# Performance work log

Hardware: AMD Instinct MI355X
Metric: run time of the kernel (lower is better)

The kernel has to match this reference:

```python
import jax, jax.numpy as jnp
import numpy as np

LEVELS = 16
BASE_RES = 16.0
MAX_RES = 2048.0
MAX_PARAMS = 2 ** 19
FEAT = 2
LOG_B = np.log(MAX_RES / BASE_RES) / (LEVELS - 1)
PRIMES = np.array([1, 2654435761, 805459861], dtype=np.uint32)


def level_meta():
    # Replays HashEncoder.__init__ offset/size bookkeeping.
    offsets, sizes, ress = [], [], []
    offset = 0
    begin_fast = LEVELS
    for i in range(LEVELS):
        res = int(np.ceil(BASE_RES * np.exp(i * LOG_B) - 1.0) + 1)  # grid_resolution
        full = float(res) ** 3
        aligned = int((full + 7) / 8) * 8  # align_to(full, 8)
        size = int(min(MAX_PARAMS, aligned))
        if full > size and begin_fast == LEVELS:
            begin_fast = i
        offsets.append(offset)
        sizes.append(size)
        ress.append(res)
        offset += size
    return offsets, sizes, ress, begin_fast, offset


OFFSETS, SIZES, RESS, BEGIN_FAST, TOTAL = level_meta()


def setup_inputs():
    key = jax.random.key(0)
    k1, k2 = jax.random.split(key)
    B = 2_000_000
    positions = jax.random.uniform(k1, (B, 3), dtype=jnp.float32)  # xyz in [0,1)
    table = jax.random.uniform(k2, (TOTAL, FEAT), dtype=jnp.float32,
                               minval=-1e-4, maxval=1e-4)
    return {"positions": positions, "table": table}


def _encode(positions, table):
    outs = []
    for level in range(LEVELS):  # fixed small structural loop (16 levels)
        scale = np.float32(BASE_RES * np.exp(level * LOG_B) - 1.0)  # grid_scale
        res = RESS[level]
        pos = positions * scale + 0.5          # [B,3]
        grid_f = jnp.floor(pos)
        frac = pos - grid_f                    # [B,3] trilinear fractions
        grid = grid_f.astype(jnp.uint32)
        acc = jnp.zeros((positions.shape[0], FEAT), dtype=jnp.float32)
        for corner in range(8):                # 8 cube corners (static unroll)
            sel = np.array([(corner >> d) & 1 for d in range(3)], dtype=np.uint32)
            pg = grid + sel                    # [B,3] uint32 corner coords
            w = jnp.prod(jnp.where(sel.astype(bool), frac, 1.0 - frac), axis=-1)  # [B]
            if level < BEGIN_FAST:
                # dense 'under_hash': x + y*res + z*res^2 (uint32 wraparound ok)
                strides = np.array([1, res, res * res], dtype=np.uint32)
                h = jnp.sum(pg * strides, axis=-1, dtype=jnp.uint32)
            else:
                # spatial 'fast_hash': xor of coord*prime with uint32 wraparound
                h = (pg[:, 0] * PRIMES[0]) ^ (pg[:, 1] * PRIMES[1]) ^ (pg[:, 2] * PRIMES[2])
            idx = (h % np.uint32(SIZES[level])).astype(jnp.int32) + OFFSETS[level]
            acc = acc + w[:, None] * table[idx]  # irregular gather [B,FEAT]
        outs.append(acc)
    # matches output_embedding[i, level].view(-1, levels*feat): level-major, feat inner
    return jnp.concatenate(outs, axis=-1)  # [B, LEVELS*FEAT]


def reference(positions, table):
    return _encode(positions, table)
```

## Files before the change

kernel.cpp:

```cpp
#include <hip/hip_runtime.h>
#include <math.h>

#define NLEVELS 16
#define BEGIN_FAST 5
#define P2 2654435761u
#define P3 805459861u
#define FAST_MASK 524287u
#define DENSE_TOTAL 330952u

constexpr unsigned kRes[NLEVELS] = {16u, 23u, 31u, 43u, 59u, 81u, 112u, 154u, 213u, 295u, 407u, 562u, 777u, 1073u, 1483u, 2048u};
constexpr unsigned kSize[NLEVELS] = {
    4096u, 12168u, 29792u, 79512u, 205384u,
    524288u, 524288u, 524288u, 524288u, 524288u, 524288u,
    524288u, 524288u, 524288u, 524288u, 524288u};
constexpr unsigned kOffset[NLEVELS] = {
    0u,       4096u,    16264u,   46056u,   125568u,  330952u,
    855240u,  1379528u, 1903816u, 2428104u, 2952392u, 3476680u,
    4000968u, 4525256u, 5049544u, 5573832u};

struct Scales {
    float s[NLEVELS];
};

typedef float fvec2 __attribute__((ext_vector_type(2)));
typedef float fvec4 __attribute__((ext_vector_type(4)));
typedef unsigned uvec4 __attribute__((ext_vector_type(4)));

__device__ __forceinline__ unsigned bfpack(float a, float b) {
    unsigned ua = __float_as_uint(a);
    unsigned ub = __float_as_uint(b);
    ua = (ua + 0x7FFFu + ((ua >> 16) & 1u)) >> 16;
    ub = (ub + 0x7FFFu + ((ub >> 16) & 1u)) & 0xFFFF0000u;
    return ua | ub;
}
__device__ __forceinline__ float bf_lo(unsigned e) { return __uint_as_float(e << 16); }
__device__ __forceinline__ float bf_hi(unsigned e) { return __uint_as_float(e & 0xFFFF0000u); }

__global__ __launch_bounds__(256) void convert_quad_kernel(
    const float2* __restrict__ table,
    uvec4* __restrict__ Q,
    int total)
{
    int j = blockIdx.x * 256 + threadIdx.x;
    if (j >= total) return;
    int l = 0;
    if (j >= (int)kOffset[1]) l = 1;
    if (j >= (int)kOffset[2]) l = 2;
    if (j >= (int)kOffset[3]) l = 3;
    if (j >= (int)kOffset[4]) l = 4;
    const unsigned size = kSize[l];
    const unsigned res = kRes[l];
    const unsigned jl = (unsigned)j - kOffset[l];
    unsigned j1 = jl + 1u;        if (j1 >= size) j1 -= size;
    unsigned jy = jl + res;       if (jy >= size) jy -= size;
    unsigned jy1 = jy + 1u;       if (jy1 >= size) jy1 -= size;
    const float2 t0 = table[kOffset[l] + jl];
    const float2 t1 = table[kOffset[l] + j1];
    const float2 t2 = table[kOffset[l] + jy];
    const float2 t3 = table[kOffset[l] + jy1];
    uvec4 r = {bfpack(t0.x, t0.y), bfpack(t1.x, t1.y),
               bfpack(t2.x, t2.y), bfpack(t3.x, t3.y)};
    __builtin_nontemporal_store(r, Q + j);
}

__global__ __launch_bounds__(256) void fine_level_kernel(
    const float* __restrict__ positions,
    const float2* __restrict__ tab,
    float2* __restrict__ wsl,
    int B, float s)
{
    int p = blockIdx.x * 256 + threadIdx.x;
    if (p >= B) return;

    const float x = __builtin_nontemporal_load(positions + 3 * p + 0);
    const float y = __builtin_nontemporal_load(positions + 3 * p + 1);
    const float z = __builtin_nontemporal_load(positions + 3 * p + 2);

    const float px = x * s + 0.5f;
    const float py = y * s + 0.5f;
    const float pz = z * s + 0.5f;
    const float flx = floorf(px), fly = floorf(py), flz = floorf(pz);
    const float rx = px - flx, ry = py - fly, rz = pz - flz;
    const unsigned gx = (unsigned)flx;
    const unsigned gy = (unsigned)fly;
    const unsigned gz = (unsigned)flz;
    const float wx0 = 1.0f - rx, wy0 = 1.0f - ry, wz0 = 1.0f - rz;

    const unsigned hy0 = gy * P2, hy1 = hy0 + P2;
    const unsigned hz0 = gz * P3, hz1 = hz0 + P3;

    float ax = 0.0f, ay = 0.0f;
#pragma unroll
    for (int c = 0; c < 8; ++c) {
        const unsigned cx = (unsigned)(c & 1);
        const unsigned cy = (unsigned)((c >> 1) & 1);
        const unsigned cz = (unsigned)((c >> 2) & 1);
        const float w = (cx ? rx : wx0) * (cy ? ry : wy0) * (cz ? rz : wz0);
        const unsigned h = (gx + cx) ^ (cy ? hy1 : hy0) ^ (cz ? hz1 : hz0);
        const float2 t = tab[h & FAST_MASK];
        ax += w * t.x;
        ay += w * t.y;
    }
    fvec2 r = {ax, ay};
    __builtin_nontemporal_store(r, reinterpret_cast<fvec2*>(wsl) + p);
}

__global__ __launch_bounds__(256) void dense_merge_kernel(
    const float* __restrict__ positions,
    const uvec4* __restrict__ Q,
    const float2* __restrict__ fws,
    float* __restrict__ out,
    int B, Scales sc)
{
    const int p = blockIdx.x * 256 + threadIdx.x;
    if (p >= B) return;

    const float x = __builtin_nontemporal_load(positions + 3 * p + 0);
    const float y = __builtin_nontemporal_load(positions + 3 * p + 1);
    const float z = __builtin_nontemporal_load(positions + 3 * p + 2);

    float o[2 * NLEVELS];

#pragma unroll
    for (int l = 0; l < BEGIN_FAST; ++l) {
        const float s = sc.s[l];
        const float px = x * s + 0.5f;
        const float py = y * s + 0.5f;
        const float pz = z * s + 0.5f;
        const float flx = floorf(px), fly = floorf(py), flz = floorf(pz);
        const float rx = px - flx, ry = py - fly, rz = pz - flz;
        const unsigned gx = (unsigned)flx;
        const unsigned gy = (unsigned)fly;
        const unsigned gz = (unsigned)flz;
        const float wx0 = 1.0f - rx, wy0 = 1.0f - ry, wz0 = 1.0f - rz;

        const uvec4* tabQ = Q + kOffset[l];
        const unsigned res = kRes[l];
        const unsigned res2 = res * res;
        const unsigned h0 = gx + gy * res + gz * res2;

        float ax = 0.0f, ay = 0.0f;
#pragma unroll
        for (int cz = 0; cz < 2; ++cz) {
            const float wz = cz ? rz : wz0;
            const unsigned idx = (h0 + (unsigned)cz * res2) % kSize[l];
            const uvec4 q = tabQ[idx];
            ax += wz * (wy0 * (wx0 * bf_lo(q.x) + rx * bf_lo(q.y)) +
                        ry  * (wx0 * bf_lo(q.z) + rx * bf_lo(q.w)));
            ay += wz * (wy0 * (wx0 * bf_hi(q.x) + rx * bf_hi(q.y)) +
                        ry  * (wx0 * bf_hi(q.z) + rx * bf_hi(q.w)));
        }
        o[2 * l + 0] = ax;
        o[2 * l + 1] = ay;
    }

#pragma unroll
    for (int l = BEGIN_FAST; l < NLEVELS; ++l) {
        const fvec2 v = __builtin_nontemporal_load(
            reinterpret_cast<const fvec2*>(fws) + (size_t)(l - BEGIN_FAST) * (size_t)B + p);
        o[2 * l + 0] = v.x;
        o[2 * l + 1] = v.y;
    }

    float* op = out + (size_t)p * (2 * NLEVELS);
#pragma unroll
    for (int i = 0; i < 8; ++i) {
        fvec4 v = {o[4 * i + 0], o[4 * i + 1], o[4 * i + 2], o[4 * i + 3]};
        *(reinterpret_cast<fvec4*>(op) + i) = v;
    }
}

__global__ __launch_bounds__(256) void hash_encode_kernel(
    const float* __restrict__ positions,
    const float2* __restrict__ table,
    float* __restrict__ out,
    int B, Scales sc)
{
    int p = blockIdx.x * 256 + threadIdx.x;
    if (p >= B) return;

    const float x = positions[3 * p + 0];
    const float y = positions[3 * p + 1];
    const float z = positions[3 * p + 2];

    float o[2 * NLEVELS];

#pragma unroll
    for (int l = 0; l < NLEVELS; ++l) {
        const float s = sc.s[l];
        const float px = x * s + 0.5f;
        const float py = y * s + 0.5f;
        const float pz = z * s + 0.5f;
        const float flx = floorf(px), fly = floorf(py), flz = floorf(pz);
        const float rx = px - flx, ry = py - fly, rz = pz - flz;
        const unsigned gx = (unsigned)flx;
        const unsigned gy = (unsigned)fly;
        const unsigned gz = (unsigned)flz;
        const float wx0 = 1.0f - rx, wy0 = 1.0f - ry, wz0 = 1.0f - rz;

        float ax = 0.0f, ay = 0.0f;
#pragma unroll
        for (int c = 0; c < 8; ++c) {
            const unsigned cx = (unsigned)(c & 1);
            const unsigned cy = (unsigned)((c >> 1) & 1);
            const unsigned cz = (unsigned)((c >> 2) & 1);
            const unsigned pgx = gx + cx;
            const unsigned pgy = gy + cy;
            const unsigned pgz = gz + cz;
            const float w = (cx ? rx : wx0) * (cy ? ry : wy0) * (cz ? rz : wz0);
            unsigned h;
            if (l < BEGIN_FAST) {
                h = pgx + pgy * kRes[l] + pgz * (kRes[l] * kRes[l]);
            } else {
                h = pgx ^ (pgy * P2) ^ (pgz * P3);
            }
            const unsigned idx = (h % kSize[l]) + kOffset[l];
            const float2 t = table[idx];
            ax += w * t.x;
            ay += w * t.y;
        }
        o[2 * l + 0] = ax;
        o[2 * l + 1] = ay;
    }

    float* op = out + (size_t)p * (2 * NLEVELS);
#pragma unroll
    for (int i = 0; i < 8; ++i) {
        fvec4 v = {o[4 * i + 0], o[4 * i + 1], o[4 * i + 2], o[4 * i + 3]};
        *(reinterpret_cast<fvec4*>(op) + i) = v;
    }
}

extern "C" void kernel_launch(void* const* d_in, const int* in_sizes, int n_in,
                              void* d_out, int out_size, void* d_ws, size_t ws_size,
                              hipStream_t stream) {
    const float* positions = (const float*)d_in[0];
    const float2* table = (const float2*)d_in[1];
    float* out = (float*)d_out;

    const int B = in_sizes[0] / 3;

    Scales sc;
    const double log_b = log(2048.0 / 16.0) / (NLEVELS - 1);
    for (int l = 0; l < NLEVELS; ++l) {
        sc.s[l] = (float)(16.0 * exp((double)l * log_b) - 1.0);
    }

    const int blocks = (B + 255) / 256;

    const size_t fws_bytes = 11u * (size_t)B * sizeof(float2);
    const size_t Q_bytes = (size_t)DENSE_TOTAL * sizeof(uvec4);
    const size_t ws_need = fws_bytes + Q_bytes;

    if (ws_size >= ws_need) {
        float2* fws = (float2*)d_ws;
        uvec4* Q = (uvec4*)((char*)d_ws + fws_bytes);

        convert_quad_kernel<<<((int)DENSE_TOTAL + 255) / 256, 256, 0, stream>>>(
            table, Q, (int)DENSE_TOTAL);

        for (int l = BEGIN_FAST; l < NLEVELS; ++l) {
            fine_level_kernel<<<blocks, 256, 0, stream>>>(
                positions, table + kOffset[l],
                fws + (size_t)(l - BEGIN_FAST) * (size_t)B, B, sc.s[l]);
        }
        dense_merge_kernel<<<blocks, 256, 0, stream>>>(positions, Q, fws, out, B, sc);
    } else {
        hash_encode_kernel<<<blocks, 256, 0, stream>>>(positions, table, out, B, sc);
    }
}
```

Baseline: 813.4 us.

## Split dense levels into per-level kernels and fuse last fine level into merge

The five dense levels now run as separate templated kernels, so each one only touches a small per-level quad table that can stay resident in cache, instead of one merge kernel gathering from all five tables at once. Each dense level writes its two features as a packed bf16 pair to workspace. The finest hash level is computed directly inside the merge kernel, which removes one intermediate write and read. In exchange, positions are read in five extra launches, extra launch overhead is added, and dense-level outputs are rounded to bf16, which costs precision.

```diff
diff --git a/kernel.cpp b/kernel.cpp
--- a/kernel.cpp
+++ b/kernel.cpp
@@ -105,62 +105,104 @@
     __builtin_nontemporal_store(r, reinterpret_cast<fvec2*>(wsl) + p);
 }
 
-__global__ __launch_bounds__(256) void dense_merge_kernel(
+template<int L>
+__global__ __launch_bounds__(256) void dense_level_kernel(
     const float* __restrict__ positions,
-    const uvec4* __restrict__ Q,
-    const float2* __restrict__ fws,
-    float* __restrict__ out,
-    int B, Scales sc)
-{
-    const int p = blockIdx.x * 256 + threadIdx.x;
+    const uvec4* __restrict__ Qs,
+    unsigned* __restrict__ dwsl,
+    int B, float s)
+{
+    int p = blockIdx.x * 256 + threadIdx.x;
     if (p >= B) return;
 
     const float x = __builtin_nontemporal_load(positions + 3 * p + 0);
     const float y = __builtin_nontemporal_load(positions + 3 * p + 1);
     const float z = __builtin_nontemporal_load(positions + 3 * p + 2);
 
+    const float px = x * s + 0.5f;
+    const float py = y * s + 0.5f;
+    const float pz = z * s + 0.5f;
+    const float flx = floorf(px), fly = floorf(py), flz = floorf(pz);
+    const float rx = px - flx, ry = py - fly, rz = pz - flz;
+    const unsigned gx = (unsigned)flx;
+    const unsigned gy = (unsigned)fly;
+    const unsigned gz = (unsigned)flz;
+    const float wx0 = 1.0f - rx, wy0 = 1.0f - ry, wz0 = 1.0f - rz;
+
+    const unsigned res = kRes[L];
+    const unsigned res2 = res * res;
+    const unsigned h0 = gx + gy * res + gz * res2;
+
+    float ax = 0.0f, ay = 0.0f;
+#pragma unroll
+    for (int cz = 0; cz < 2; ++cz) {
+        const float wz = cz ? rz : wz0;
+        const unsigned idx = (h0 + (unsigned)cz * res2) % kSize[L];
+        const uvec4 q = Qs[idx];
+        ax += wz * (wy0 * (wx0 * bf_lo(q.x) + rx * bf_lo(q.y)) +
+                    ry  * (wx0 * bf_lo(q.z) + rx * bf_lo(q.w)));
+        ay += wz * (wy0 * (wx0 * bf_hi(q.x) + rx * bf_hi(q.y)) +
+                    ry  * (wx0 * bf_hi(q.z) + rx * bf_hi(q.w)));
+    }
+    __builtin_nontemporal_store(bfpack(ax, ay), dwsl + p);
+}
+
+__global__ __launch_bounds__(256) void merge_final_kernel(
+    const float* __restrict__ positions,
+    const float2* __restrict__ tab15,
+    const unsigned* __restrict__ dws,
+    const float2* __restrict__ fws,
+    float* __restrict__ out,
+    int B, float s15)
+{
+    const int p = blockIdx.x * 256 + threadIdx.x;
+    if (p >= B) return;
+
+    const float x = __builtin_nontemporal_load(positions + 3 * p + 0);
+    const float y = __builtin_nontemporal_load(positions + 3 * p + 1);
+    const float z = __builtin_nontemporal_load(positions + 3 * p + 2);
+
+    const float px = x * s15 + 0.5f;
+    const float py = y * s15 + 0.5f;
+    const float pz = z * s15 + 0.5f;
+    const float flx = floorf(px), fly = floorf(py), flz = floorf(pz);
+    const float rx = px - flx, ry = py - fly, rz = pz - flz;
+    const unsigned gx = (unsigned)flx;
+    const unsigned gy = (unsigned)fly;
+    const unsigned gz = (unsigned)flz;
+    const float wx0 = 1.0f - rx, wy0 = 1.0f - ry, wz0 = 1.0f - rz;
+    const unsigned hy0 = gy * P2, hy1 = hy0 + P2;
+    const unsigned hz0 = gz * P3, hz1 = hz0 + P3;
+
+    float a15x = 0.0f, a15y = 0.0f;
+#pragma unroll
+    for (int c = 0; c < 8; ++c) {
+        const unsigned cx = (unsigned)(c & 1);
+        const unsigned cy = (unsigned)((c >> 1) & 1);
+        const unsigned cz = (unsigned)((c >> 2) & 1);
+        const float w = (cx ? rx : wx0) * (cy ? ry : wy0) * (cz ? rz : wz0);
+        const unsigned h = (gx + cx) ^ (cy ? hy1 : hy0) ^ (cz ? hz1 : hz0);
+        const float2 t = tab15[h & FAST_MASK];
+        a15x += w * t.x;
+        a15y += w * t.y;
+    }
+
     float o[2 * NLEVELS];
-
 #pragma unroll
     for (int l = 0; l < BEGIN_FAST; ++l) {
-        const float s = sc.s[l];
-        const float px = x * s + 0.5f;
-        const float py = y * s + 0.5f;
-        const float pz = z * s + 0.5f;
-        const float flx = floorf(px), fly = floorf(py), flz = floorf(pz);
-        const float rx = px - flx, ry = py - fly, rz = pz - flz;
-        const unsigned gx = (unsigned)flx;
-        const unsigned gy = (unsigned)fly;
-        const unsigned gz = (unsigned)flz;
-        const float wx0 = 1.0f - rx, wy0 = 1.0f - ry, wz0 = 1.0f - rz;
-
-        const uvec4* tabQ = Q + kOffset[l];
-        const unsigned res = kRes[l];
-        const unsigned res2 = res * res;
-        const unsigned h0 = gx + gy * res + gz * res2;
-
-        float ax = 0.0f, ay = 0.0f;
-#pragma unroll
-        for (int cz = 0; cz < 2; ++cz) {
-            const float wz = cz ? rz : wz0;
-            const unsigned idx = (h0 + (unsigned)cz * res2) % kSize[l];
-            const uvec4 q = tabQ[idx];
-            ax += wz * (wy0 * (wx0 * bf_lo(q.x) + rx * bf_lo(q.y)) +
-                        ry  * (wx0 * bf_lo(q.z) + rx * bf_lo(q.w)));
-            ay += wz * (wy0 * (wx0 * bf_hi(q.x) + rx * bf_hi(q.y)) +
-                        ry  * (wx0 * bf_hi(q.z) + rx * bf_hi(q.w)));
-        }
-        o[2 * l + 0] = ax;
-        o[2 * l + 1] = ay;
-    }
-
-#pragma unroll
-    for (int l = BEGIN_FAST; l < NLEVELS; ++l) {
+        const unsigned v = __builtin_nontemporal_load(dws + (size_t)l * (size_t)B + p);
+        o[2 * l + 0] = bf_lo(v);
+        o[2 * l + 1] = bf_hi(v);
+    }
+#pragma unroll
+    for (int l = BEGIN_FAST; l < NLEVELS - 1; ++l) {
         const fvec2 v = __builtin_nontemporal_load(
             reinterpret_cast<const fvec2*>(fws) + (size_t)(l - BEGIN_FAST) * (size_t)B + p);
         o[2 * l + 0] = v.x;
         o[2 * l + 1] = v.y;
     }
+    o[30] = a15x;
+    o[31] = a15y;
 
     float* op = out + (size_t)p * (2 * NLEVELS);
 #pragma unroll
@@ -248,23 +290,33 @@
 
     const int blocks = (B + 255) / 256;
 
-    const size_t fws_bytes = 11u * (size_t)B * sizeof(float2);
+    const size_t dws_bytes = 5u * (size_t)B * sizeof(unsigned);
+    const size_t fws_bytes = 10u * (size_t)B * sizeof(float2);
     const size_t Q_bytes = (size_t)DENSE_TOTAL * sizeof(uvec4);
-    const size_t ws_need = fws_bytes + Q_bytes;
+    const size_t ws_need = dws_bytes + fws_bytes + Q_bytes;
 
     if (ws_size >= ws_need) {
-        float2* fws = (float2*)d_ws;
-        uvec4* Q = (uvec4*)((char*)d_ws + fws_bytes);
+        unsigned* dws = (unsigned*)d_ws;
+        float2* fws = (float2*)((char*)d_ws + dws_bytes);
+        uvec4* Q = (uvec4*)((char*)d_ws + dws_bytes + fws_bytes);
 
         convert_quad_kernel<<<((int)DENSE_TOTAL + 255) / 256, 256, 0, stream>>>(
             table, Q, (int)DENSE_TOTAL);
 
-        for (int l = BEGIN_FAST; l < NLEVELS; ++l) {
+        dense_level_kernel<0><<<blocks, 256, 0, stream>>>(positions, Q + kOffset[0], dws + 0 * (size_t)B, B, sc.s[0]);
+        dense_level_kernel<1><<<blocks, 256, 0, stream>>>(positions, Q + kOffset[1], dws + 1 * (size_t)B, B, sc.s[1]);
+        dense_level_kernel<2><<<blocks, 256, 0, stream>>>(positions, Q + kOffset[2], dws + 2 * (size_t)B, B, sc.s[2]);
+        dense_level_kernel<3><<<blocks, 256, 0, stream>>>(positions, Q + kOffset[3], dws + 3 * (size_t)B, B, sc.s[3]);
+        dense_level_kernel<4><<<blocks, 256, 0, stream>>>(positions, Q + kOffset[4], dws + 4 * (size_t)B, B, sc.s[4]);
+
+        for (int l = BEGIN_FAST; l < NLEVELS - 1; ++l) {
             fine_level_kernel<<<blocks, 256, 0, stream>>>(
                 positions, table + kOffset[l],
                 fws + (size_t)(l - BEGIN_FAST) * (size_t)B, B, sc.s[l]);
         }
-        dense_merge_kernel<<<blocks, 256, 0, stream>>>(positions, Q, fws, out, B, sc);
+
+        merge_final_kernel<<<blocks, 256, 0, stream>>>(
+            positions, table + kOffset[15], dws, fws, out, B, sc.s[15]);
     } else {
         hash_encode_kernel<<<blocks, 256, 0, stream>>>(positions, table, out, B, sc);
     }
```

Result: no change. 826.5 us (+1.6%).
